# Performance work log

Measured on AMD Instinct MI355X. Metric: run time of the kernel, lower is better.

Reference implementation:

```python
import jax, jax.numpy as jnp
import numpy as np

N_NODES = 50000
N_EDGES = 800000
N_GRAPHS = 128
IN_CH, HIDDEN, OUT_CH = 16, 64, 2


def gcn_conv(x, src, dst, W, b, n_nodes):
    """GCNConv: add self-loops, sym-normalized adjacency scatter-add, linear."""
    h = x @ W  # [N, H]
    loop = jnp.arange(n_nodes, dtype=src.dtype)
    s = jnp.concatenate([src, loop])  # [E+N]
    d = jnp.concatenate([dst, loop])
    deg = jax.ops.segment_sum(jnp.ones_like(d, dtype=h.dtype), d, num_segments=n_nodes)
    dinv = jnp.where(deg > 0, jax.lax.rsqrt(deg), 0.0)  # deg^{-1/2}
    norm = dinv[s] * dinv[d]  # [E+N]
    msg = h[s] * norm[:, None]  # gather + scale, [E+N, H]
    out = jax.ops.segment_sum(msg, d, num_segments=n_nodes)  # scatter-add
    return out + b


def global_mean_pool(x, batch, n_graphs):
    sums = jax.ops.segment_sum(x, batch, num_segments=n_graphs)
    cnts = jax.ops.segment_sum(jnp.ones((x.shape[0],), x.dtype), batch, num_segments=n_graphs)
    return sums / jnp.maximum(cnts, 1.0)[:, None]


def setup_inputs() -> dict:
    key = jax.random.key(0)
    ks = jax.random.split(key, 10)
    x = jax.random.normal(ks[0], (N_NODES, IN_CH), dtype=jnp.float32)
    edge_index = jax.random.randint(ks[1], (2, N_EDGES), 0, N_NODES, dtype=jnp.int64)
    batch = jnp.sort(jax.random.randint(ks[2], (N_NODES,), 0, N_GRAPHS, dtype=jnp.int64))
    def glorot(k, shp):
        lim = float(np.sqrt(6.0 / (shp[0] + shp[1])))
        return jax.random.uniform(k, shp, jnp.float32, -lim, lim)
    W1 = glorot(ks[3], (IN_CH, HIDDEN))
    b1 = jnp.zeros((HIDDEN,), jnp.float32)
    W2 = glorot(ks[4], (HIDDEN, HIDDEN))
    b2 = jnp.zeros((HIDDEN,), jnp.float32)
    Wc = glorot(ks[5], (HIDDEN, OUT_CH))
    bc = jnp.zeros((OUT_CH,), jnp.float32)
    return {"x": x, "edge_index": edge_index, "batch": batch,
            "W1": W1, "b1": b1, "W2": W2, "b2": b2, "Wc": Wc, "bc": bc}


def reference(x, edge_index, batch, W1, b1, W2, b2, Wc, bc):
    src, dst = edge_index[0], edge_index[1]
    n = x.shape[0]
    h = jax.nn.relu(gcn_conv(x, src, dst, W1, b1, n))
    # dropout p=0.3 is identity in eval mode
    h = jax.nn.relu(gcn_conv(h, src, dst, W2, b2, n))
    g = global_mean_pool(h, batch, N_GRAPHS)  # [G, H]
    return g @ Wc + bc  # [G, out_channels]
```

## Files before the change

### kernel.cpp

```cpp
#include <hip/hip_runtime.h>
#include <hip/hip_bf16.h>

#define N_NODES 50000
#define N_EDGES 800000
#define N_GRAPHS 128
#define IN_CH 16
#define HIDDEN 64
#define OUT_CH 2

#define BSHIFT 7
#define BNODES 128
#define NB ((N_NODES + BNODES - 1) / BNODES)
#define ECHUNK 4096
#define EB ((N_EDGES + ECHUNK - 1) / ECHUNK)
#define SLEN (NB * EB)
#define SCHUNK 1024
#define NSB ((SLEN + SCHUNK - 1) / SCHUNK)
#define MAXK 12
#define WT1_LD 18
#define AGG_LD 72

typedef __attribute__((ext_vector_type(8))) short bf16x8;
typedef __attribute__((ext_vector_type(4))) float f32x4;

__device__ __forceinline__ float bf2f(unsigned short u) {
    return __uint_as_float(((unsigned)u) << 16);
}
__device__ __forceinline__ unsigned short f2bf(float f) {
    __hip_bfloat16 h = __float2bfloat16(f);
    return *reinterpret_cast<unsigned short*>(&h);
}


__global__ void bucket_hist_kernel(const int* __restrict__ dst, int* __restrict__ bh,
                                   float* __restrict__ sums, float* __restrict__ cntg) {
    __shared__ int lh[NB];
    int t = threadIdx.x;
    if (blockIdx.x == 0) {
        for (int i = t; i < N_GRAPHS * HIDDEN; i += 256) sums[i] = 0.0f;
        if (t < N_GRAPHS) cntg[t] = 0.0f;
    }
    for (int i = t; i < NB; i += 256) lh[i] = 0;
    __syncthreads();
    int base = blockIdx.x * ECHUNK;
    for (int i = t; i < ECHUNK; i += 256) {
        int e = base + i;
        if (e < N_EDGES) {
            int d = dst[e];
            if ((unsigned)d < N_NODES) atomicAdd(&lh[d >> BSHIFT], 1);
        }
    }
    __syncthreads();
    for (int i = t; i < NB; i += 256) bh[i * EB + blockIdx.x] = lh[i];
}

__global__ void scan_part_kernel(const int* __restrict__ a, int* __restrict__ bsum) {
    __shared__ int s[256];
    int t = threadIdx.x;
    int ebase = blockIdx.x * SCHUNK + t * 4;
    int v = 0;
    if (ebase + 3 < SLEN) {
        int4 c = *(const int4*)&a[ebase];
        v = c.x + c.y + c.z + c.w;
    } else {
        for (int k = 0; k < 4; k++) {
            int i = ebase + k;
            if (i < SLEN) v += a[i];
        }
    }
    s[t] = v;
    __syncthreads();
    for (int off = 128; off > 0; off >>= 1) {
        if (t < off) s[t] += s[t + off];
        __syncthreads();
    }
    if (t == 0) bsum[blockIdx.x] = s[0];
}

__global__ void scan_apply_kernel(const int* __restrict__ a, const int* __restrict__ bsum,
                                  int* __restrict__ boff) {
    __shared__ int sb[256];
    __shared__ int st[256];
    int t = threadIdx.x;
    sb[t] = (t < NSB) ? bsum[t] : 0;
    __syncthreads();
    for (int off = 1; off < 256; off <<= 1) {
        int u = (t >= off) ? sb[t - off] : 0;
        __syncthreads();
        sb[t] += u;
        __syncthreads();
    }
    int blockOff = (blockIdx.x > 0) ? sb[blockIdx.x - 1] : 0;

    int ebase = blockIdx.x * SCHUNK + t * 4;
    int c0 = 0, c1 = 0, c2 = 0, c3 = 0;
    bool full = (ebase + 3 < SLEN);
    if (full) {
        int4 c = *(const int4*)&a[ebase];
        c0 = c.x; c1 = c.y; c2 = c.z; c3 = c.w;
    } else {
        if (ebase < SLEN) c0 = a[ebase];
        if (ebase + 1 < SLEN) c1 = a[ebase + 1];
        if (ebase + 2 < SLEN) c2 = a[ebase + 2];
    }
    int tsum = c0 + c1 + c2 + c3;
    st[t] = tsum;
    __syncthreads();
    for (int off = 1; off < 256; off <<= 1) {
        int u = (t >= off) ? st[t - off] : 0;
        __syncthreads();
        st[t] += u;
        __syncthreads();
    }
    int p = blockOff + st[t] - tsum;
    if (full) {
        int4 o;
        o.x = p; o.y = p + c0; o.z = p + c0 + c1; o.w = p + c0 + c1 + c2;
        *(int4*)&boff[ebase] = o;
    } else {
        if (ebase < SLEN) boff[ebase] = p;
        if (ebase + 1 < SLEN) boff[ebase + 1] = p + c0;
        if (ebase + 2 < SLEN) boff[ebase + 2] = p + c0 + c1;
        if (ebase + 3 < SLEN) boff[ebase + 3] = p + c0 + c1 + c2;
    }
}

__global__ void bucket_scatter_kernel(const int* __restrict__ src, const int* __restrict__ dst,
                                      const int* __restrict__ boff, int2* __restrict__ pairs) {
    __shared__ int lcnt[NB];
    __shared__ int goff[NB];
    int t = threadIdx.x;
    for (int i = t; i < NB; i += 256) {
        lcnt[i] = 0;
        goff[i] = boff[i * EB + blockIdx.x];
    }
    __syncthreads();
    int base = blockIdx.x * ECHUNK;
    for (int i = t; i < ECHUNK; i += 256) {
        int e = base + i;
        if (e < N_EDGES) {
            int d = dst[e];
            if ((unsigned)d < N_NODES) {
                int b = d >> BSHIFT;
                int r = atomicAdd(&lcnt[b], 1);
                int2 p;
                p.x = src[e];
                p.y = d;
                pairs[goff[b] + r] = p;
            }
        }
    }
}

__global__ void bucket_csr_kernel(const int2* __restrict__ pairs, const int* __restrict__ boff,
                                  int* __restrict__ csr, int* __restrict__ rowptr,
                                  int* __restrict__ cnt_node, float* __restrict__ dinv) {
    __shared__ int lcnt[BNODES];
    __shared__ int ls[BNODES];
    __shared__ int lrow[BNODES];
    int b = blockIdx.x;
    int t = threadIdx.x;
    if (t < BNODES) lcnt[t] = 0;
    __syncthreads();
    int bstart = boff[b * EB];
    int bend = (b + 1 < NB) ? boff[(b + 1) * EB] : N_EDGES;
    int K = bend - bstart;
    int myn[MAXK], myr[MAXK], mys[MAXK];
#pragma unroll
    for (int k = 0; k < MAXK; k++) {
        int i = k * 256 + t;
        if (i < K) {
            int2 p = pairs[bstart + i];
            int nl = p.y & (BNODES - 1);
            mys[k] = p.x;
            myn[k] = nl;
            myr[k] = atomicAdd(&lcnt[nl], 1);
        }
    }
    __syncthreads();
    if (t < BNODES) ls[t] = lcnt[t];
    __syncthreads();
    for (int off = 1; off < BNODES; off <<= 1) {
        int u = (t >= off && t < BNODES) ? ls[t - off] : 0;
        __syncthreads();
        if (t < BNODES) ls[t] += u;
        __syncthreads();
    }
    if (t < BNODES) {
        int ex = ls[t] - lcnt[t];
        lrow[t] = ex;
        int n = b * BNODES + t;
        if (n < N_NODES) {
            rowptr[n] = bstart + ex;
            cnt_node[n] = lcnt[t];
            dinv[n] = rsqrtf((float)(lcnt[t] + 1));
        }
    }
    __syncthreads();
#pragma unroll
    for (int k = 0; k < MAXK; k++) {
        int i = k * 256 + t;
        if (i < K) csr[bstart + lrow[myn[k]] + myr[k]] = mys[k];
    }
}


__global__ void fused_l1_kernel(const float* __restrict__ x, const int* __restrict__ csr_src,
                                const int* __restrict__ rowptr, const int* __restrict__ cnt,
                                const float* __restrict__ dinv, const float* __restrict__ W,
                                const float* __restrict__ b, __hip_bfloat16* __restrict__ h) {
    __shared__ float sWT[HIDDEN * WT1_LD];
    __shared__ float sx[16 * IN_CH];
    int t = threadIdx.x;
    for (int i = t; i < IN_CH * HIDDEN; i += 256) {
        int k = i >> 6, c = i & 63;
        sWT[c * WT1_LD + k] = W[i];
    }

    int n0 = blockIdx.x * 16;
    int w = t >> 6;
    int lane = t & 63;
    int e16 = lane >> 2;
    int cc = (lane & 3) * 4;

    for (int q = 0; q < 4; q++) {
        int row = w * 4 + q;
        int n = n0 + row;
        if (n >= N_NODES) break;
        int len = cnt[n];
        int start = rowptr[n];
        float4 acc = make_float4(0.f, 0.f, 0.f, 0.f);
        for (int i = e16; i < len; i += 16) {
            int s = csr_src[start + i];
            float dv = dinv[s];
            float4 xv = *(const float4*)&x[s * IN_CH + cc];
            acc.x += dv * xv.x; acc.y += dv * xv.y;
            acc.z += dv * xv.z; acc.w += dv * xv.w;
        }
#pragma unroll
        for (int m = 4; m <= 32; m <<= 1) {
            acc.x += __shfl_xor(acc.x, m, 64);
            acc.y += __shfl_xor(acc.y, m, 64);
            acc.z += __shfl_xor(acc.z, m, 64);
            acc.w += __shfl_xor(acc.w, m, 64);
        }
        if (lane < 4) {
            float dn = dinv[n];
            float4 xs = *(const float4*)&x[n * IN_CH + cc];
            float4 v;
            v.x = dn * acc.x + dn * dn * xs.x;
            v.y = dn * acc.y + dn * dn * xs.y;
            v.z = dn * acc.z + dn * dn * xs.z;
            v.w = dn * acc.w + dn * dn * xs.w;
            *(float4*)&sx[row * IN_CH + cc] = v;
        }
    }
    __syncthreads();

    int r = w;
    int c = t & 63;
    float bias = b[c];
#pragma unroll
    for (int nb = 0; nb < 4; nb++) {
        int row = nb * 4 + r;
        int n = n0 + row;
        if (n >= N_NODES) continue;
        float acch = bias;
#pragma unroll
        for (int k4 = 0; k4 < IN_CH; k4 += 4) {
            float4 a = *(const float4*)&sx[row * IN_CH + k4];
            float2 w0 = *(const float2*)&sWT[c * WT1_LD + k4];
            float2 w1 = *(const float2*)&sWT[c * WT1_LD + k4 + 2];
            acch += a.x * w0.x + a.y * w0.y + a.z * w1.x + a.w * w1.y;
        }
        float v = acch > 0.0f ? acch : 0.0f;
        h[n * HIDDEN + c] = __float2bfloat16(dinv[n] * v);
    }
}


__global__ void fused_l2_kernel(const __hip_bfloat16* __restrict__ h, const int* __restrict__ csr_src,
                                const int* __restrict__ rowptr, const int* __restrict__ cnt,
                                const float* __restrict__ dinv, const float* __restrict__ W,
                                const float* __restrict__ b, const int* __restrict__ batch,
                                float* __restrict__ sums, float* __restrict__ cntg) {
    __shared__ unsigned short sW[HIDDEN * AGG_LD];
    __shared__ unsigned short sagg[16 * AGG_LD];
    int t = threadIdx.x;
    for (int i = t; i < HIDDEN * HIDDEN; i += 256) {
        int k = i >> 6, c = i & 63;
        sW[c * AGG_LD + k] = f2bf(W[i]);
    }

    int n0 = blockIdx.x * 16;
    int w = t >> 6;
    int lane = t & 63;
    int e4 = lane >> 4;
    int cc = (lane & 15) * 4;
    const unsigned short* hu = (const unsigned short*)h;

    for (int q = 0; q < 4; q++) {
        int row = w * 4 + q;
        int n = n0 + row;
        int len = cnt[n];
        int start = rowptr[n];
        float4 acc = make_float4(0.f, 0.f, 0.f, 0.f);
        int i = e4;
        for (; i + 12 < len; i += 16) {
            int s0 = csr_src[start + i];
            int s1 = csr_src[start + i + 4];
            int s2 = csr_src[start + i + 8];
            int s3 = csr_src[start + i + 12];
            ushort4 a0 = *(const ushort4*)&hu[s0 * HIDDEN + cc];
            ushort4 a1 = *(const ushort4*)&hu[s1 * HIDDEN + cc];
            ushort4 a2 = *(const ushort4*)&hu[s2 * HIDDEN + cc];
            ushort4 a3 = *(const ushort4*)&hu[s3 * HIDDEN + cc];
            acc.x += (bf2f(a0.x) + bf2f(a1.x)) + (bf2f(a2.x) + bf2f(a3.x));
            acc.y += (bf2f(a0.y) + bf2f(a1.y)) + (bf2f(a2.y) + bf2f(a3.y));
            acc.z += (bf2f(a0.z) + bf2f(a1.z)) + (bf2f(a2.z) + bf2f(a3.z));
            acc.w += (bf2f(a0.w) + bf2f(a1.w)) + (bf2f(a2.w) + bf2f(a3.w));
        }
        for (; i < len; i += 4) {
            int s0 = csr_src[start + i];
            ushort4 a0 = *(const ushort4*)&hu[s0 * HIDDEN + cc];
            acc.x += bf2f(a0.x);
            acc.y += bf2f(a0.y);
            acc.z += bf2f(a0.z);
            acc.w += bf2f(a0.w);
        }
        acc.x += __shfl_xor(acc.x, 16, 64);
        acc.y += __shfl_xor(acc.y, 16, 64);
        acc.z += __shfl_xor(acc.z, 16, 64);
        acc.w += __shfl_xor(acc.w, 16, 64);
        acc.x += __shfl_xor(acc.x, 32, 64);
        acc.y += __shfl_xor(acc.y, 32, 64);
        acc.z += __shfl_xor(acc.z, 32, 64);
        acc.w += __shfl_xor(acc.w, 32, 64);
        if (lane < 16) {
            ushort4 sv = *(const ushort4*)&hu[n * HIDDEN + cc];
            float dn = dinv[n];
            ushort4 o;
            o.x = f2bf(dn * (acc.x + bf2f(sv.x)));
            o.y = f2bf(dn * (acc.y + bf2f(sv.y)));
            o.z = f2bf(dn * (acc.z + bf2f(sv.z)));
            o.w = f2bf(dn * (acc.w + bf2f(sv.w)));
            *(ushort4*)&sagg[row * AGG_LD + cc] = o;
        }
    }
    __syncthreads();

    int quad = lane >> 4;
    int col = lane & 15;
    int cch = w * 16 + col;
    bf16x8 a0 = *(const bf16x8*)&sagg[col * AGG_LD + quad * 8];
    bf16x8 a1 = *(const bf16x8*)&sagg[col * AGG_LD + 32 + quad * 8];
    bf16x8 b0 = *(const bf16x8*)&sW[cch * AGG_LD + quad * 8];
    bf16x8 b1 = *(const bf16x8*)&sW[cch * AGG_LD + 32 + quad * 8];
    f32x4 d = {0.f, 0.f, 0.f, 0.f};
    d = __builtin_amdgcn_mfma_f32_16x16x32_bf16(a0, b0, d, 0, 0, 0);
    d = __builtin_amdgcn_mfma_f32_16x16x32_bf16(a1, b1, d, 0, 0, 0);
    float bias = b[cch];
    float v[4];
#pragma unroll
    for (int r = 0; r < 4; r++) {
        float z = d[r] + bias;
        v[r] = z > 0.0f ? z : 0.0f;
    }

    int glo = batch[n0];
    int ghi = batch[n0 + 15];
    if (glo == ghi) {
        float s4 = (v[0] + v[1]) + (v[2] + v[3]);
        s4 += __shfl_xor(s4, 16, 64);
        s4 += __shfl_xor(s4, 32, 64);
        if (quad == 0) atomicAdd(&sums[glo * HIDDEN + cch], s4);
        if (t == 0) atomicAdd(&cntg[glo], 16.0f);
    } else {
#pragma unroll
        for (int r = 0; r < 4; r++) {
            int g = batch[n0 + quad * 4 + r];
            if ((unsigned)g < N_GRAPHS) atomicAdd(&sums[g * HIDDEN + cch], v[r]);
        }
        if (w == 0 && col == 0) {
#pragma unroll
            for (int r = 0; r < 4; r++) {
                int g = batch[n0 + quad * 4 + r];
                if ((unsigned)g < N_GRAPHS) atomicAdd(&cntg[g], 1.0f);
            }
        }
    }
}


__global__ void head_kernel(const float* __restrict__ sums, const float* __restrict__ cntg,
                            const float* __restrict__ Wc, const float* __restrict__ bc,
                            float* __restrict__ out) {
    int t = blockIdx.x * blockDim.x + threadIdx.x;
    if (t >= N_GRAPHS * OUT_CH) return;
    int g = t >> 1;
    int o = t & 1;
    float inv = 1.0f / fmaxf(cntg[g], 1.0f);
    float acc = bc[o];
#pragma unroll
    for (int k = 0; k < HIDDEN; k++) acc += sums[g * HIDDEN + k] * inv * Wc[k * OUT_CH + o];
    out[t] = acc;
}


extern "C" void kernel_launch(void* const* d_in, const int* in_sizes, int n_in,
                              void* d_out, int out_size, void* d_ws, size_t ws_size,
                              hipStream_t stream) {
    const float* x  = (const float*)d_in[0];
    const int* ei   = (const int*)d_in[1];
    const int* bat  = (const int*)d_in[2];
    const float* W1 = (const float*)d_in[3];
    const float* b1 = (const float*)d_in[4];
    const float* W2 = (const float*)d_in[5];
    const float* b2 = (const float*)d_in[6];
    const float* Wc = (const float*)d_in[7];
    const float* bc = (const float*)d_in[8];
    float* out = (float*)d_out;

    const int* src = ei;
    const int* dst = ei + N_EDGES;

    char* ws = (char*)d_ws;
    size_t off = 0;
    auto carve = [&](size_t nbytes) {
        char* p = ws + off;
        off += (nbytes + 255) & ~(size_t)255;
        return p;
    };
    float* sums     = (float*)carve(N_GRAPHS * HIDDEN * sizeof(float));
    float* cntg     = (float*)carve(N_GRAPHS * sizeof(float));
    int*   bh       = (int*)carve((size_t)SLEN * sizeof(int));
    int*   bsum     = (int*)carve(NSB * sizeof(int));
    int*   boff     = (int*)carve((size_t)SLEN * sizeof(int));
    int2*  pairs    = (int2*)carve((size_t)N_EDGES * sizeof(int2));
    int*   csr      = (int*)carve((size_t)N_EDGES * sizeof(int));
    int*   rowptr   = (int*)carve(N_NODES * sizeof(int));
    int*   cnt_node = (int*)carve(N_NODES * sizeof(int));
    float* dinv     = (float*)carve(N_NODES * sizeof(float));
    __hip_bfloat16* bufA = (__hip_bfloat16*)carve((size_t)N_NODES * HIDDEN * sizeof(__hip_bfloat16));
    (void)ws_size;

    const int node16Blk = (N_NODES + 15) / 16;

    bucket_hist_kernel<<<EB, 256, 0, stream>>>(dst, bh, sums, cntg);
    scan_part_kernel<<<NSB, 256, 0, stream>>>(bh, bsum);
    scan_apply_kernel<<<NSB, 256, 0, stream>>>(bh, bsum, boff);
    bucket_scatter_kernel<<<EB, 256, 0, stream>>>(src, dst, boff, pairs);
    bucket_csr_kernel<<<NB, 256, 0, stream>>>(pairs, boff, csr, rowptr, cnt_node, dinv);

    fused_l1_kernel<<<node16Blk, 256, 0, stream>>>(x, csr, rowptr, cnt_node, dinv, W1, b1, bufA);
    fused_l2_kernel<<<node16Blk, 256, 0, stream>>>(bufA, csr, rowptr, cnt_node, dinv, W2, b2,
                                                   bat, sums, cntg);
    head_kernel<<<1, 256, 0, stream>>>(sums, cntg, Wc, bc, out);
}
```

Baseline: 178.1 us.

## Pack edge pairs into one int, pretranspose W2 once, hoist row loads, mask tail

Edge (src,dst) pairs are packed into a single 32-bit int (src shifted left by 7, node-local index in the low bits), halving the scatter/CSR intermediate traffic. The bf16 transpose of W2 is built once by block 1 of the histogram kernel, so each layer-2 block copies it into shared memory with vector loads instead of converting it itself. Both fused layers prefetch rowptr and count for their four rows before the gather loops, and the layer-2 gather loop is rewritten as a uniform 4-way unrolled loop that clamps and masks the tail in place of a separate remainder loop. The masked loop issues redundant clamped loads at the tail, and the packing assumes src fits in 25 bits.

```diff
diff --git a/kernel.cpp b/kernel.cpp
--- a/kernel.cpp
+++ b/kernel.cpp
@@ -19,6 +19,7 @@
 #define MAXK 12
 #define WT1_LD 18
 #define AGG_LD 72
+#define W2T_ENT (HIDDEN * AGG_LD)
 
 typedef __attribute__((ext_vector_type(8))) short bf16x8;
 typedef __attribute__((ext_vector_type(4))) float f32x4;
@@ -33,12 +34,19 @@
 
 
 __global__ void bucket_hist_kernel(const int* __restrict__ dst, int* __restrict__ bh,
-                                   float* __restrict__ sums, float* __restrict__ cntg) {
+                                   float* __restrict__ sums, float* __restrict__ cntg,
+                                   const float* __restrict__ W2, unsigned short* __restrict__ w2t) {
     __shared__ int lh[NB];
     int t = threadIdx.x;
     if (blockIdx.x == 0) {
         for (int i = t; i < N_GRAPHS * HIDDEN; i += 256) sums[i] = 0.0f;
         if (t < N_GRAPHS) cntg[t] = 0.0f;
+    }
+    if (blockIdx.x == 1) {
+        for (int i = t; i < HIDDEN * HIDDEN; i += 256) {
+            int k = i >> 6, c = i & 63;
+            w2t[c * AGG_LD + k] = f2bf(W2[i]);
+        }
     }
     for (int i = t; i < NB; i += 256) lh[i] = 0;
     __syncthreads();
@@ -126,7 +134,7 @@
 }
 
 __global__ void bucket_scatter_kernel(const int* __restrict__ src, const int* __restrict__ dst,
-                                      const int* __restrict__ boff, int2* __restrict__ pairs) {
+                                      const int* __restrict__ boff, int* __restrict__ pairs) {
     __shared__ int lcnt[NB];
     __shared__ int goff[NB];
     int t = threadIdx.x;
@@ -143,16 +151,13 @@
             if ((unsigned)d < N_NODES) {
                 int b = d >> BSHIFT;
                 int r = atomicAdd(&lcnt[b], 1);
-                int2 p;
-                p.x = src[e];
-                p.y = d;
-                pairs[goff[b] + r] = p;
+                pairs[goff[b] + r] = (src[e] << BSHIFT) | (d & (BNODES - 1));
             }
         }
     }
 }
 
-__global__ void bucket_csr_kernel(const int2* __restrict__ pairs, const int* __restrict__ boff,
+__global__ void bucket_csr_kernel(const int* __restrict__ pairs, const int* __restrict__ boff,
                                   int* __restrict__ csr, int* __restrict__ rowptr,
                                   int* __restrict__ cnt_node, float* __restrict__ dinv) {
     __shared__ int lcnt[BNODES];
@@ -165,16 +170,14 @@
     int bstart = boff[b * EB];
     int bend = (b + 1 < NB) ? boff[(b + 1) * EB] : N_EDGES;
     int K = bend - bstart;
-    int myn[MAXK], myr[MAXK], mys[MAXK];
+    int myp[MAXK], myr[MAXK];
 #pragma unroll
     for (int k = 0; k < MAXK; k++) {
         int i = k * 256 + t;
         if (i < K) {
-            int2 p = pairs[bstart + i];
-            int nl = p.y & (BNODES - 1);
-            mys[k] = p.x;
-            myn[k] = nl;
-            myr[k] = atomicAdd(&lcnt[nl], 1);
+            int p = pairs[bstart + i];
+            myp[k] = p;
+            myr[k] = atomicAdd(&lcnt[p & (BNODES - 1)], 1);
         }
     }
     __syncthreads();
@@ -200,7 +203,7 @@
 #pragma unroll
     for (int k = 0; k < MAXK; k++) {
         int i = k * 256 + t;
-        if (i < K) csr[bstart + lrow[myn[k]] + myr[k]] = mys[k];
+        if (i < K) csr[bstart + lrow[myp[k] & (BNODES - 1)] + myr[k]] = myp[k] >> BSHIFT;
     }
 }
 
@@ -223,12 +226,19 @@
     int e16 = lane >> 2;
     int cc = (lane & 3) * 4;
 
+    int lens[4], starts[4];
+#pragma unroll
+    for (int q = 0; q < 4; q++) {
+        int n = n0 + w * 4 + q;
+        lens[q] = cnt[n];
+        starts[q] = rowptr[n];
+    }
+
     for (int q = 0; q < 4; q++) {
         int row = w * 4 + q;
         int n = n0 + row;
-        if (n >= N_NODES) break;
-        int len = cnt[n];
-        int start = rowptr[n];
+        int len = lens[q];
+        int start = starts[q];
         float4 acc = make_float4(0.f, 0.f, 0.f, 0.f);
         for (int i = e16; i < len; i += 16) {
             int s = csr_src[start + i];
@@ -281,15 +291,20 @@
 
 __global__ void fused_l2_kernel(const __hip_bfloat16* __restrict__ h, const int* __restrict__ csr_src,
                                 const int* __restrict__ rowptr, const int* __restrict__ cnt,
-                                const float* __restrict__ dinv, const float* __restrict__ W,
+                                const float* __restrict__ dinv, const unsigned short* __restrict__ w2t,
                                 const float* __restrict__ b, const int* __restrict__ batch,
                                 float* __restrict__ sums, float* __restrict__ cntg) {
-    __shared__ unsigned short sW[HIDDEN * AGG_LD];
+    __shared__ unsigned short sW[W2T_ENT];
     __shared__ unsigned short sagg[16 * AGG_LD];
     int t = threadIdx.x;
-    for (int i = t; i < HIDDEN * HIDDEN; i += 256) {
-        int k = i >> 6, c = i & 63;
-        sW[c * AGG_LD + k] = f2bf(W[i]);
+    {
+        const uint4* wp = (const uint4*)w2t;
+        uint4* sWv = (uint4*)sW;
+#pragma unroll
+        for (int i = 0; i < 3; i++) {
+            int idx = i * 256 + t;
+            if (idx < W2T_ENT / 8) sWv[idx] = wp[idx];
+        }
     }
 
     int n0 = blockIdx.x * 16;
@@ -299,34 +314,36 @@
     int cc = (lane & 15) * 4;
     const unsigned short* hu = (const unsigned short*)h;
 
+    int lens[4], starts[4];
+#pragma unroll
+    for (int q = 0; q < 4; q++) {
+        int n = n0 + w * 4 + q;
+        lens[q] = cnt[n];
+        starts[q] = rowptr[n];
+    }
+
     for (int q = 0; q < 4; q++) {
         int row = w * 4 + q;
         int n = n0 + row;
-        int len = cnt[n];
-        int start = rowptr[n];
+        int len = lens[q];
+        int start = starts[q];
         float4 acc = make_float4(0.f, 0.f, 0.f, 0.f);
-        int i = e4;
-        for (; i + 12 < len; i += 16) {
-            int s0 = csr_src[start + i];
-            int s1 = csr_src[start + i + 4];
-            int s2 = csr_src[start + i + 8];
-            int s3 = csr_src[start + i + 12];
-            ushort4 a0 = *(const ushort4*)&hu[s0 * HIDDEN + cc];
-            ushort4 a1 = *(const ushort4*)&hu[s1 * HIDDEN + cc];
-            ushort4 a2 = *(const ushort4*)&hu[s2 * HIDDEN + cc];
-            ushort4 a3 = *(const ushort4*)&hu[s3 * HIDDEN + cc];
-            acc.x += (bf2f(a0.x) + bf2f(a1.x)) + (bf2f(a2.x) + bf2f(a3.x));
-            acc.y += (bf2f(a0.y) + bf2f(a1.y)) + (bf2f(a2.y) + bf2f(a3.y));
-            acc.z += (bf2f(a0.z) + bf2f(a1.z)) + (bf2f(a2.z) + bf2f(a3.z));
-            acc.w += (bf2f(a0.w) + bf2f(a1.w)) + (bf2f(a2.w) + bf2f(a3.w));
-        }
-        for (; i < len; i += 4) {
-            int s0 = csr_src[start + i];
-            ushort4 a0 = *(const ushort4*)&hu[s0 * HIDDEN + cc];
-            acc.x += bf2f(a0.x);
-            acc.y += bf2f(a0.y);
-            acc.z += bf2f(a0.z);
-            acc.w += bf2f(a0.w);
+        int last = len - 1;
+        int iters = (len + 15) >> 4;
+        for (int m = 0; m < iters; m++) {
+            int base = m * 16 + e4;
+#pragma unroll
+            for (int k = 0; k < 4; k++) {
+                int j = base + 4 * k;
+                int jj = j <= last ? j : last;
+                float msk = j <= last ? 1.0f : 0.0f;
+                int s = csr_src[start + jj];
+                ushort4 a = *(const ushort4*)&hu[s * HIDDEN + cc];
+                acc.x += msk * bf2f(a.x);
+                acc.y += msk * bf2f(a.y);
+                acc.z += msk * bf2f(a.z);
+                acc.w += msk * bf2f(a.w);
+            }
         }
         acc.x += __shfl_xor(acc.x, 16, 64);
         acc.y += __shfl_xor(acc.y, 16, 64);
@@ -433,10 +450,11 @@
     };
     float* sums     = (float*)carve(N_GRAPHS * HIDDEN * sizeof(float));
     float* cntg     = (float*)carve(N_GRAPHS * sizeof(float));
+    unsigned short* w2t = (unsigned short*)carve(W2T_ENT * sizeof(unsigned short));
     int*   bh       = (int*)carve((size_t)SLEN * sizeof(int));
     int*   bsum     = (int*)carve(NSB * sizeof(int));
     int*   boff     = (int*)carve((size_t)SLEN * sizeof(int));
-    int2*  pairs    = (int2*)carve((size_t)N_EDGES * sizeof(int2));
+    int*   pairs    = (int*)carve((size_t)N_EDGES * sizeof(int));
     int*   csr      = (int*)carve((size_t)N_EDGES * sizeof(int));
     int*   rowptr   = (int*)carve(N_NODES * sizeof(int));
     int*   cnt_node = (int*)carve(N_NODES * sizeof(int));
@@ -446,14 +464,14 @@
 
     const int node16Blk = (N_NODES + 15) / 16;
 
-    bucket_hist_kernel<<<EB, 256, 0, stream>>>(dst, bh, sums, cntg);
+    bucket_hist_kernel<<<EB, 256, 0, stream>>>(dst, bh, sums, cntg, W2, w2t);
     scan_part_kernel<<<NSB, 256, 0, stream>>>(bh, bsum);
     scan_apply_kernel<<<NSB, 256, 0, stream>>>(bh, bsum, boff);
     bucket_scatter_kernel<<<EB, 256, 0, stream>>>(src, dst, boff, pairs);
     bucket_csr_kernel<<<NB, 256, 0, stream>>>(pairs, boff, csr, rowptr, cnt_node, dinv);
 
     fused_l1_kernel<<<node16Blk, 256, 0, stream>>>(x, csr, rowptr, cnt_node, dinv, W1, b1, bufA);
-    fused_l2_kernel<<<node16Blk, 256, 0, stream>>>(bufA, csr, rowptr, cnt_node, dinv, W2, b2,
+    fused_l2_kernel<<<node16Blk, 256, 0, stream>>>(bufA, csr, rowptr, cnt_node, dinv, w2t, b2,
                                                    bat, sums, cntg);
     head_kernel<<<1, 256, 0, stream>>>(sums, cntg, Wc, bc, out);
 }
```

Result: faster. 171.9 us (-3.5%).
